# Optimization experiments

Measured on AMD Instinct MI355X. Metric: run time of the kernel, lower is better.

Reference implementation:

```python
import jax, jax.numpy as jnp
import numpy as np
import math

INPUT_SIZE = 128  # feature dim D, from init_kwargs

def setup_inputs() -> dict:
    key = jax.random.key(0)
    k1, k2 = jax.random.split(key)
    B, N, D = 4, 4096, INPUT_SIZE
    inp = jax.random.normal(k1, (B, N, D), dtype=jnp.float32)
    adj = jax.random.randint(k2, (B, N, N), 0, 2, dtype=jnp.int32)
    return {"input": inp, "adj": adj}

def reference(input, adj):
    # scores: [B, N, N] = X X^T / sqrt(D)
    scores = jnp.matmul(input, jnp.swapaxes(input, 1, 2)) / math.sqrt(INPUT_SIZE)
    neg = jnp.asarray(-1e12, dtype=scores.dtype)
    masked = jnp.where(adj > 0, scores, neg)
    attention = jax.nn.softmax(masked, axis=2)
    out_hid = jnp.matmul(attention, input)  # [B, N, D]
    return out_hid
```

## Files before the change

### kernel.cpp

```cpp
#include <hip/hip_runtime.h>
#include <hip/hip_bf16.h>


#define NN 4096
#define DD 128
#define BK 128

#define XB_OFF   0
#define XBT_OFF  32768
#define P_OFF    65536
#define P_WSTRIDE 1280
#define LDS_BYTES (P_OFF + 16 * P_WSTRIDE)

typedef __attribute__((ext_vector_type(8))) short bf16x8;
typedef __attribute__((ext_vector_type(4))) float f32x4;

static __device__ __forceinline__ unsigned f2bf(float f) {
    union { float f; unsigned u; } v; v.f = f;
    return (v.u + 0x7fffu + ((v.u >> 16) & 1u)) >> 16;
}

static __device__ __forceinline__ void gl_lds16(const void* g, void* l) {
    __builtin_amdgcn_global_load_lds(
        (const __attribute__((address_space(1))) unsigned*)g,
        (__attribute__((address_space(3))) unsigned*)l, 16, 0, 0);
}

__global__ __launch_bounds__(256)
void gat_prep(const float* __restrict__ X, unsigned short* __restrict__ xb,
              unsigned short* __restrict__ xbt) {
    __shared__ unsigned short tile[64][132];
    const int t = threadIdx.x;
    const int b  = blockIdx.x >> 6;
    const int kc = blockIdx.x & 63;
    const float* src = X + ((size_t)b * NN + kc * 64) * DD;
    unsigned short* xbo = xb + ((size_t)b * NN + kc * 64) * DD;

    #pragma unroll
    for (int it = 0; it < 8; ++it) {
        int f = it * 256 + t;
        int k = f >> 5, d4 = (f & 31) * 4;
        float4 v = *(const float4*)(src + (size_t)f * 4);
        uint2 pk;
        pk.x = f2bf(v.x) | (f2bf(v.y) << 16);
        pk.y = f2bf(v.z) | (f2bf(v.w) << 16);
        *(uint2*)(xbo + (size_t)f * 4) = pk;
        *(uint2*)(&tile[k][d4]) = pk;
    }
    __syncthreads();
    const int d = t >> 1, kb0 = (t & 1) * 32;
    unsigned short* dst = xbt + (size_t)b * DD * NN + (size_t)d * NN + kc * 64 + kb0;
    #pragma unroll
    for (int c = 0; c < 4; ++c) {
        union { uint4 o; unsigned short e[8]; } u;
        #pragma unroll
        for (int j = 0; j < 8; ++j) u.e[j] = tile[kb0 + c * 8 + j][d];
        *(uint4*)(dst + c * 8) = u.o;
    }
}

__global__ __launch_bounds__(1024, 4)
void gat_fused(const unsigned short* __restrict__ xb,
               const unsigned short* __restrict__ xbt,
               const int* __restrict__ adj,
               float* __restrict__ out) {
    extern __shared__ char lds[];
    const int t = threadIdx.x;
    const int w = t >> 6, l = t & 63;
    const int h = l >> 4, l16 = l & 15;
    const int rw = w & 3;
    const int kh = w >> 2;

    const int bid  = blockIdx.x;
    const int b    = bid >> 6;
    const int row0 = (bid & 63) * 64;
    const int qbase = row0 + rw * 16;

    const char* xb_b  = (const char*)(xb  + (size_t)b * NN * DD);
    const char* xbt_b = (const char*)(xbt + (size_t)b * DD * NN);
    const int*  Ag    = adj + (size_t)b * NN * NN;
    float*      Og    = out + (size_t)b * NN * DD;

    bf16x8 qfrag[4];
    {
        const char* qp = xb_b + (size_t)(qbase + l16) * DD * 2;
        #pragma unroll
        for (int ds = 0; ds < 4; ++ds)
            qfrag[ds] = *(const bf16x8*)(qp + ds * 64 + h * 16);
    }

    const int c = l16;
    int off_xb[2], off_xbt[2];
    #pragma unroll
    for (int j = 0; j < 2; ++j) {
        int r0 = w * 8 + 4 * j + h;
        off_xb[j]  = r0 * 256        + ((c ^ (r0 & 7)) * 16);
        off_xbt[j] = r0 * (NN * 2)   + ((c ^ (r0 & 7)) * 16);
    }
    char* ldsXb  = lds + XB_OFF  + w * 2048;
    char* ldsXbt = lds + XBT_OFF + w * 2048;
    char* pw     = lds + P_OFF   + w * P_WSTRIDE;
    const int kbase = kh * 32;

    f32x4 oacc[8];
    #pragma unroll
    for (int cf = 0; cf < 8; ++cf) oacc[cf] = (f32x4){0.f, 0.f, 0.f, 0.f};
    float psum = 0.f;

    for (int kt = 0; kt < NN / BK; ++kt) {
        const int key0 = kt * BK;

        int4 av[2];
        #pragma unroll
        for (int f = 0; f < 2; ++f)
            av[f] = *(const int4*)(Ag + (size_t)(qbase + l16) * NN
                                      + key0 + kbase + f * 16 + 4 * h);

        __syncthreads();

        #pragma unroll
        for (int j = 0; j < 2; ++j) {
            gl_lds16(xb_b  + key0 * 256 + off_xb[j],  ldsXb  + j * 1024);
            gl_lds16(xbt_b + key0 * 2   + off_xbt[j], ldsXbt + j * 1024);
        }
        __syncthreads();

        f32x4 sacc[2];
        #pragma unroll
        for (int f = 0; f < 2; ++f) {
            sacc[f] = (f32x4){0.f, 0.f, 0.f, 0.f};
            const int krow = kbase + f * 16 + l16;
            const char* rp = lds + XB_OFF + krow * 256;
            const int sw = krow & 7;
            #pragma unroll
            for (int ds = 0; ds < 4; ++ds) {
                bf16x8 kf_ = *(const bf16x8*)(rp + ((h + 4 * ds) ^ sw) * 16);
                sacc[f] = __builtin_amdgcn_mfma_f32_16x16x32_bf16(
                    kf_, qfrag[ds], sacc[f], 0, 0, 0);
            }
        }

        #pragma unroll
        for (int f = 0; f < 2; ++f) {
            const float SC = 0.08838834764831845f;
            float p0 = (av[f].x > 0) ? __expf(sacc[f][0] * SC) : 0.f;
            float p1 = (av[f].y > 0) ? __expf(sacc[f][1] * SC) : 0.f;
            float p2 = (av[f].z > 0) ? __expf(sacc[f][2] * SC) : 0.f;
            float p3 = (av[f].w > 0) ? __expf(sacc[f][3] * SC) : 0.f;
            psum += p0 + p1 + p2 + p3;
            uint2 pk;
            pk.x = f2bf(p0) | (f2bf(p1) << 16);
            pk.y = f2bf(p2) | (f2bf(p3) << 16);
            *(uint2*)(pw + l16 * 80 + f * 32 + h * 8) = pk;
        }

        bf16x8 pfrag = *(const bf16x8*)(pw + l16 * 80 + h * 16);
        #pragma unroll
        for (int cf = 0; cf < 8; ++cf) {
            const int vrow = l16 + 16 * cf;
            bf16x8 vfrag = *(const bf16x8*)(lds + XBT_OFF + vrow * 256
                                + (((4 * kh + h) ^ (vrow & 7)) * 16));
            oacc[cf] = __builtin_amdgcn_mfma_f32_16x16x32_bf16(
                pfrag, vfrag, oacc[cf], 0, 0, 0);
        }
    }

    psum += __shfl_xor(psum, 16, 64);
    psum += __shfl_xor(psum, 32, 64);

    __syncthreads();
    float* psarea = (float*)(lds + P_OFF);
    if (l < 16) psarea[(kh * 4 + rw) * 16 + l] = psum;
    float* oa = (float*)lds;
    if (kh >= 2) {
        float* dst = oa + ((kh - 2) * 4 + rw) * 2048;
        #pragma unroll
        for (int cf = 0; cf < 8; ++cf)
            #pragma unroll
            for (int r = 0; r < 4; ++r)
                dst[(4 * h + r) * 128 + l16 + 16 * cf] = oacc[cf][r];
    }
    __syncthreads();
    if (kh < 2) {
        const float* sp = oa + (kh * 4 + rw) * 2048;
        #pragma unroll
        for (int cf = 0; cf < 8; ++cf)
            #pragma unroll
            for (int r = 0; r < 4; ++r)
                oacc[cf][r] += sp[(4 * h + r) * 128 + l16 + 16 * cf];
    }
    __syncthreads();
    if (kh == 1) {
        float* dst = oa + rw * 2048;
        #pragma unroll
        for (int cf = 0; cf < 8; ++cf)
            #pragma unroll
            for (int r = 0; r < 4; ++r)
                dst[(4 * h + r) * 128 + l16 + 16 * cf] = oacc[cf][r];
    }
    __syncthreads();
    if (kh == 0) {
        const float* sp = oa + rw * 2048;
        float inv[4];
        #pragma unroll
        for (int r = 0; r < 4; ++r) {
            int q = 4 * h + r;
            float tot = psarea[rw * 16 + q]        + psarea[(4 + rw) * 16 + q]
                      + psarea[(8 + rw) * 16 + q]  + psarea[(12 + rw) * 16 + q];
            inv[r] = 1.0f / tot;
        }
        float* dst = oa + rw * 2048;
        #pragma unroll
        for (int cf = 0; cf < 8; ++cf)
            #pragma unroll
            for (int r = 0; r < 4; ++r)
                dst[(4 * h + r) * 128 + l16 + 16 * cf] =
                    (oacc[cf][r] + sp[(4 * h + r) * 128 + l16 + 16 * cf]) * inv[r];
    }
    __syncthreads();
    const float4* oaf4 = (const float4*)oa;
    float4* dstf4 = (float4*)(Og + (size_t)row0 * DD);
    dstf4[t]        = oaf4[t];
    dstf4[t + 1024] = oaf4[t + 1024];
}

extern "C" void kernel_launch(void* const* d_in, const int* in_sizes, int n_in,
                              void* d_out, int out_size, void* d_ws, size_t ws_size,
                              hipStream_t stream) {
    const float* X   = (const float*)d_in[0];
    const int*   adj = (const int*)d_in[1];
    float*       out = (float*)d_out;
    unsigned short* xb  = (unsigned short*)d_ws;
    unsigned short* xbt = xb + (size_t)4 * NN * DD * 2;
    xbt = xb + (size_t)4 * NN * DD;

    hipFuncSetAttribute((const void*)gat_fused,
                        hipFuncAttributeMaxDynamicSharedMemorySize, LDS_BYTES);
    gat_prep<<<dim3(256), dim3(256), 0, stream>>>(X, xb, xbt);
    gat_fused<<<dim3(256), dim3(1024), LDS_BYTES, stream>>>(xb, xbt, adj, out);
}
```

Baseline: 428.6 us.

## Double-buffer K/V tiles in LDS and prefetch adjacency one step ahead

Splits the LDS staging area into two buffers so the next key tile's global-to-LDS loads are issued before computing on the current tile, and loads the adjacency values for the next step ahead of time. Each iteration now needs one barrier plus a vmcnt wait instead of two __syncthreads. This is meant to hide global load latency behind the MFMA work. LDS use roughly doubles to about 148 KB per block, and the wait relies on a hand-set vmcnt count.

```diff
diff --git a/kernel.cpp b/kernel.cpp
--- a/kernel.cpp
+++ b/kernel.cpp
@@ -5,10 +5,11 @@
 #define NN 4096
 #define DD 128
 #define BK 128
-
-#define XB_OFF   0
-#define XBT_OFF  32768
-#define P_OFF    65536
+#define NT (NN / BK)
+
+#define XBT_REL 32768
+#define BUF1_OFF 65536
+#define P_OFF 131072
 #define P_WSTRIDE 1280
 #define LDS_BYTES (P_OFF + 16 * P_WSTRIDE)
 
@@ -75,6 +76,7 @@
     const int b    = bid >> 6;
     const int row0 = (bid & 63) * 64;
     const int qbase = row0 + rw * 16;
+    const int kbase = kh * 32;
 
     const char* xb_b  = (const char*)(xb  + (size_t)b * NN * DD);
     const char* xbt_b = (const char*)(xbt + (size_t)b * DD * NN);
@@ -89,88 +91,108 @@
             qfrag[ds] = *(const bf16x8*)(qp + ds * 64 + h * 16);
     }
 
-    const int c = l16;
     int off_xb[2], off_xbt[2];
     #pragma unroll
     for (int j = 0; j < 2; ++j) {
         int r0 = w * 8 + 4 * j + h;
-        off_xb[j]  = r0 * 256        + ((c ^ (r0 & 7)) * 16);
-        off_xbt[j] = r0 * (NN * 2)   + ((c ^ (r0 & 7)) * 16);
-    }
-    char* ldsXb  = lds + XB_OFF  + w * 2048;
-    char* ldsXbt = lds + XBT_OFF + w * 2048;
-    char* pw     = lds + P_OFF   + w * P_WSTRIDE;
-    const int kbase = kh * 32;
+        off_xb[j]  = r0 * 256      + ((l16 ^ (r0 & 7)) * 16);
+        off_xbt[j] = r0 * (NN * 2) + ((l16 ^ (r0 & 7)) * 16);
+    }
+    char* bufA = lds;
+    char* bufB = lds + BUF1_OFF;
+    char* pw   = lds + P_OFF + w * P_WSTRIDE;
+
+    const int* arow = Ag + (size_t)(qbase + l16) * NN + kbase + 4 * h;
+
+    #pragma unroll
+    for (int j = 0; j < 2; ++j) {
+        gl_lds16(xb_b  + off_xb[j],  bufA + w * 2048 + j * 1024);
+        gl_lds16(xbt_b + off_xbt[j], bufA + XBT_REL + w * 2048 + j * 1024);
+    }
+    int4 avA0 = *(const int4*)(arow);
+    int4 avA1 = *(const int4*)(arow + 16);
 
     f32x4 oacc[8];
     #pragma unroll
     for (int cf = 0; cf < 8; ++cf) oacc[cf] = (f32x4){0.f, 0.f, 0.f, 0.f};
     float psum = 0.f;
 
-    for (int kt = 0; kt < NN / BK; ++kt) {
-        const int key0 = kt * BK;
-
-        int4 av[2];
-        #pragma unroll
-        for (int f = 0; f < 2; ++f)
-            av[f] = *(const int4*)(Ag + (size_t)(qbase + l16) * NN
-                                      + key0 + kbase + f * 16 + 4 * h);
-
-        __syncthreads();
-
+#define COMPUTE(BUF, AV0, AV1) do {                                            \
+    f32x4 sacc0 = (f32x4){0.f,0.f,0.f,0.f}, sacc1 = (f32x4){0.f,0.f,0.f,0.f};  \
+    {                                                                          \
+        const int krow0 = kbase + l16;                                         \
+        const int krow1 = kbase + 16 + l16;                                    \
+        const char* rp0 = (BUF) + krow0 * 256;                                 \
+        const char* rp1 = (BUF) + krow1 * 256;                                 \
+        const int sw = l16 & 7;                                                \
+        _Pragma("unroll")                                                      \
+        for (int ds = 0; ds < 4; ++ds) {                                       \
+            bf16x8 kf0 = *(const bf16x8*)(rp0 + (((h + 4*ds) ^ sw) * 16));     \
+            sacc0 = __builtin_amdgcn_mfma_f32_16x16x32_bf16(                   \
+                kf0, qfrag[ds], sacc0, 0, 0, 0);                               \
+            bf16x8 kf1 = *(const bf16x8*)(rp1 + (((h + 4*ds) ^ sw) * 16));     \
+            sacc1 = __builtin_amdgcn_mfma_f32_16x16x32_bf16(                   \
+                kf1, qfrag[ds], sacc1, 0, 0, 0);                               \
+        }                                                                      \
+    }                                                                          \
+    {                                                                          \
+        const float SC = 0.08838834764831845f;                                 \
+        float p0 = ((AV0).x > 0) ? __expf(sacc0[0] * SC) : 0.f;                \
+        float p1 = ((AV0).y > 0) ? __expf(sacc0[1] * SC) : 0.f;                \
+        float p2 = ((AV0).z > 0) ? __expf(sacc0[2] * SC) : 0.f;                \
+        float p3 = ((AV0).w > 0) ? __expf(sacc0[3] * SC) : 0.f;                \
+        psum += p0 + p1 + p2 + p3;                                             \
+        uint2 pk0; pk0.x = f2bf(p0) | (f2bf(p1) << 16);                        \
+        pk0.y = f2bf(p2) | (f2bf(p3) << 16);                                   \
+        *(uint2*)(pw + l16 * 80 + h * 8) = pk0;                                \
+        float q0 = ((AV1).x > 0) ? __expf(sacc1[0] * SC) : 0.f;                \
+        float q1 = ((AV1).y > 0) ? __expf(sacc1[1] * SC) : 0.f;                \
+        float q2 = ((AV1).z > 0) ? __expf(sacc1[2] * SC) : 0.f;                \
+        float q3 = ((AV1).w > 0) ? __expf(sacc1[3] * SC) : 0.f;                \
+        psum += q0 + q1 + q2 + q3;                                             \
+        uint2 pk1; pk1.x = f2bf(q0) | (f2bf(q1) << 16);                        \
+        pk1.y = f2bf(q2) | (f2bf(q3) << 16);                                   \
+        *(uint2*)(pw + l16 * 80 + 32 + h * 8) = pk1;                           \
+    }                                                                          \
+    {                                                                          \
+        bf16x8 pfrag = *(const bf16x8*)(pw + l16 * 80 + h * 16);               \
+        _Pragma("unroll")                                                      \
+        for (int cf = 0; cf < 8; ++cf) {                                       \
+            const int vrow = l16 + 16 * cf;                                    \
+            bf16x8 vfrag = *(const bf16x8*)((BUF) + XBT_REL + vrow * 256       \
+                              + (((4*kh + h) ^ (vrow & 7)) * 16));             \
+            oacc[cf] = __builtin_amdgcn_mfma_f32_16x16x32_bf16(                \
+                pfrag, vfrag, oacc[cf], 0, 0, 0);                              \
+        }                                                                      \
+    }                                                                          \
+} while (0)
+
+    for (int kt = 0; kt < NT - 1; ++kt) {
+        int4 avB0 = *(const int4*)(arow + (kt + 1) * BK);
+        int4 avB1 = *(const int4*)(arow + (kt + 1) * BK + 16);
+        asm volatile("s_waitcnt vmcnt(2)" ::: "memory");
+        __builtin_amdgcn_s_barrier();
         #pragma unroll
         for (int j = 0; j < 2; ++j) {
-            gl_lds16(xb_b  + key0 * 256 + off_xb[j],  ldsXb  + j * 1024);
-            gl_lds16(xbt_b + key0 * 2   + off_xbt[j], ldsXbt + j * 1024);
+            gl_lds16(xb_b  + (size_t)(kt + 1) * BK * 256 + off_xb[j],
+                     bufB + w * 2048 + j * 1024);
+            gl_lds16(xbt_b + (size_t)(kt + 1) * BK * 2 + off_xbt[j],
+                     bufB + XBT_REL + w * 2048 + j * 1024);
         }
-        __syncthreads();
-
-        f32x4 sacc[2];
-        #pragma unroll
-        for (int f = 0; f < 2; ++f) {
-            sacc[f] = (f32x4){0.f, 0.f, 0.f, 0.f};
-            const int krow = kbase + f * 16 + l16;
-            const char* rp = lds + XB_OFF + krow * 256;
-            const int sw = krow & 7;
-            #pragma unroll
-            for (int ds = 0; ds < 4; ++ds) {
-                bf16x8 kf_ = *(const bf16x8*)(rp + ((h + 4 * ds) ^ sw) * 16);
-                sacc[f] = __builtin_amdgcn_mfma_f32_16x16x32_bf16(
-                    kf_, qfrag[ds], sacc[f], 0, 0, 0);
-            }
-        }
-
-        #pragma unroll
-        for (int f = 0; f < 2; ++f) {
-            const float SC = 0.08838834764831845f;
-            float p0 = (av[f].x > 0) ? __expf(sacc[f][0] * SC) : 0.f;
-            float p1 = (av[f].y > 0) ? __expf(sacc[f][1] * SC) : 0.f;
-            float p2 = (av[f].z > 0) ? __expf(sacc[f][2] * SC) : 0.f;
-            float p3 = (av[f].w > 0) ? __expf(sacc[f][3] * SC) : 0.f;
-            psum += p0 + p1 + p2 + p3;
-            uint2 pk;
-            pk.x = f2bf(p0) | (f2bf(p1) << 16);
-            pk.y = f2bf(p2) | (f2bf(p3) << 16);
-            *(uint2*)(pw + l16 * 80 + f * 32 + h * 8) = pk;
-        }
-
-        bf16x8 pfrag = *(const bf16x8*)(pw + l16 * 80 + h * 16);
-        #pragma unroll
-        for (int cf = 0; cf < 8; ++cf) {
-            const int vrow = l16 + 16 * cf;
-            bf16x8 vfrag = *(const bf16x8*)(lds + XBT_OFF + vrow * 256
-                                + (((4 * kh + h) ^ (vrow & 7)) * 16));
-            oacc[cf] = __builtin_amdgcn_mfma_f32_16x16x32_bf16(
-                pfrag, vfrag, oacc[cf], 0, 0, 0);
-        }
-    }
+        COMPUTE(bufA, avA0, avA1);
+        char* tmp = bufA; bufA = bufB; bufB = tmp;
+        avA0 = avB0; avA1 = avB1;
+    }
+    asm volatile("s_waitcnt vmcnt(0)" ::: "memory");
+    __builtin_amdgcn_s_barrier();
+    COMPUTE(bufA, avA0, avA1);
 
     psum += __shfl_xor(psum, 16, 64);
     psum += __shfl_xor(psum, 32, 64);
 
     __syncthreads();
     float* psarea = (float*)(lds + P_OFF);
-    if (l < 16) psarea[(kh * 4 + rw) * 16 + l] = psum;
+    if (l < 16) psarea[w * 16 + l] = psum;
     float* oa = (float*)lds;
     if (kh >= 2) {
         float* dst = oa + ((kh - 2) * 4 + rw) * 2048;
@@ -205,8 +227,8 @@
         #pragma unroll
         for (int r = 0; r < 4; ++r) {
             int q = 4 * h + r;
-            float tot = psarea[rw * 16 + q]        + psarea[(4 + rw) * 16 + q]
-                      + psarea[(8 + rw) * 16 + q]  + psarea[(12 + rw) * 16 + q];
+            float tot = psarea[rw * 16 + q]       + psarea[(4 + rw) * 16 + q]
+                      + psarea[(8 + rw) * 16 + q] + psarea[(12 + rw) * 16 + q];
             inv[r] = 1.0f / tot;
         }
         float* dst = oa + rw * 2048;
@@ -222,6 +244,7 @@
     float4* dstf4 = (float4*)(Og + (size_t)row0 * DD);
     dstf4[t]        = oaf4[t];
     dstf4[t + 1024] = oaf4[t + 1024];
+#undef COMPUTE
 }
 
 extern "C" void kernel_launch(void* const* d_in, const int* in_sizes, int n_in,
@@ -231,8 +254,7 @@
     const int*   adj = (const int*)d_in[1];
     float*       out = (float*)d_out;
     unsigned short* xb  = (unsigned short*)d_ws;
-    unsigned short* xbt = xb + (size_t)4 * NN * DD * 2;
-    xbt = xb + (size_t)4 * NN * DD;
+    unsigned short* xbt = xb + (size_t)4 * NN * DD;
 
     hipFuncSetAttribute((const void*)gat_fused,
                         hipFuncAttributeMaxDynamicSharedMemorySize, LDS_BYTES);
```

After: 399.9 us. -6.7%, faster.
